# Performance work log

Hardware: AMD Instinct MI355X
Metric: run time of the kernel (lower is better)

Reference implementation:

```python
import jax, jax.numpy as jnp
import numpy as np
from jax import lax

B, C_IN, H, W = 128, 3, 256, 256
C_OUT, K = 16, 3


def setup_inputs() -> dict:
    key = jax.random.key(0)
    k1, k2, k3 = jax.random.split(key, 3)
    x = jax.random.normal(k1, (B, C_IN, H, W), dtype=jnp.float32)
    # PyTorch ConvTranspose2d weight layout: (in_channels, out_channels, kH, kW)
    weight = jax.random.normal(k2, (C_IN, C_OUT, K, K), dtype=jnp.float32) * (1.0 / np.sqrt(C_IN * K * K))
    bias = jax.random.normal(k3, (C_OUT, 1, 1), dtype=jnp.float32)
    return {"x": x, "weight": weight, "bias": bias}


def reference(x, weight, bias):
    # conv_transpose2d(stride=1, padding=0) == full correlation with spatially
    # flipped kernel, with in/out channel axes swapped to OIHW.
    k = weight.shape[-1]
    w = jnp.flip(weight, axis=(2, 3)).transpose(1, 0, 2, 3)  # [C_out, C_in, k, k]
    y = lax.conv_general_dilated(
        x, w,
        window_strides=(1, 1),
        padding=[(k - 1, k - 1), (k - 1, k - 1)],
        dimension_numbers=("NCHW", "OIHW", "NCHW"),
    )  # [B, C_out, H+k-1, W+k-1]
    y = jnp.mean(y, axis=(2, 3), keepdims=True)          # [B, C_out, 1, 1]
    y = y + bias[None]                                   # broadcast [C_out,1,1]
    y = jax.nn.logsumexp(y, axis=1, keepdims=True)       # [B, 1, 1, 1]
    y = jnp.sum(y, axis=(2, 3))                          # [B, 1]
    return y * 10.0
```

## Files before the change

### kernel.cpp

```cpp
#include <hip/hip_runtime.h>

#define BATCH   128
#define C_IN    3
#define C_OUT   16
#define HW      65536
#define F4_PER_PLANE 16384
#define THREADS 1024
#define NWAVES  (THREADS / 64)
#define F4_ITERS (F4_PER_PLANE / THREADS)

__global__ __launch_bounds__(THREADS) void fused_batch(
        const float* __restrict__ x,
        const float* __restrict__ weight,
        const float* __restrict__ bias,
        float* __restrict__ out) {
    const int b = blockIdx.x;
    const int t = threadIdx.x;
    const float4* xp = (const float4*)x + (size_t)b * (3 * F4_PER_PLANE);

    float a0 = 0.0f, a1 = 0.0f, a2 = 0.0f;
#pragma unroll
    for (int i = 0; i < F4_ITERS; ++i) {
        float4 v0 = xp[0 * F4_PER_PLANE + i * THREADS + t];
        float4 v1 = xp[1 * F4_PER_PLANE + i * THREADS + t];
        float4 v2 = xp[2 * F4_PER_PLANE + i * THREADS + t];
        a0 += (v0.x + v0.y) + (v0.z + v0.w);
        a1 += (v1.x + v1.y) + (v1.z + v1.w);
        a2 += (v2.x + v2.y) + (v2.z + v2.w);
    }

#pragma unroll
    for (int off = 32; off > 0; off >>= 1) {
        a0 += __shfl_down(a0, off, 64);
        a1 += __shfl_down(a1, off, 64);
        a2 += __shfl_down(a2, off, 64);
    }
    __shared__ float smem[NWAVES][3];
    const int lane = t & 63;
    const int wv   = t >> 6;
    if (lane == 0) { smem[wv][0] = a0; smem[wv][1] = a1; smem[wv][2] = a2; }
    __syncthreads();

    if (t == 0) {
        float S[C_IN] = {0.0f, 0.0f, 0.0f};
#pragma unroll
        for (int w = 0; w < NWAVES; ++w) {
            S[0] += smem[w][0];
            S[1] += smem[w][1];
            S[2] += smem[w][2];
        }
        const float inv_area = 1.0f / (258.0f * 258.0f);
        float m[C_OUT];
        float mmax = -1e30f;
#pragma unroll
        for (int co = 0; co < C_OUT; ++co) {
            float v = bias[co];
#pragma unroll
            for (int ci = 0; ci < C_IN; ++ci) {
                float ws9 = 0.0f;
#pragma unroll
                for (int k = 0; k < 9; ++k)
                    ws9 += weight[(ci * C_OUT + co) * 9 + k];
                v += S[ci] * ws9 * inv_area;
            }
            m[co] = v;
            mmax = fmaxf(mmax, v);
        }
        float se = 0.0f;
#pragma unroll
        for (int co = 0; co < C_OUT; ++co) se += expf(m[co] - mmax);
        out[b] = 10.0f * (logf(se) + mmax);
    }
}

extern "C" void kernel_launch(void* const* d_in, const int* in_sizes, int n_in,
                              void* d_out, int out_size, void* d_ws, size_t ws_size,
                              hipStream_t stream) {
    const float* x      = (const float*)d_in[0];
    const float* weight = (const float*)d_in[1];
    const float* bias   = (const float*)d_in[2];
    float* out = (float*)d_out;

    fused_batch<<<BATCH, THREADS, 0, stream>>>(x, weight, bias, out);
}
```

Measured before the change: 150.9 us.

## Split each batch reduction across two blocks with atomic last-block finalize

Each batch's spatial sum is now computed by two blocks, each covering half of every plane, which doubles the grid from 128 to 256 blocks. Each block writes its partial channel sums to workspace and bumps a per-batch atomic counter. The second block to arrive combines the two partials and runs the logsumexp epilogue. The goal is to fill more of the GPU's compute units for this memory-bound reduction, at the cost of an extra memset launch and atomic/fence traffic.

```diff
diff --git a/kernel.cpp b/kernel.cpp
--- a/kernel.cpp
+++ b/kernel.cpp
@@ -3,24 +3,31 @@
 #define BATCH   128
 #define C_IN    3
 #define C_OUT   16
-#define HW      65536
 #define F4_PER_PLANE 16384
 #define THREADS 1024
 #define NWAVES  (THREADS / 64)
-#define F4_ITERS (F4_PER_PLANE / THREADS)
+#define NBLK    (BATCH * 2)
+#define F4_HALF (F4_PER_PLANE / 2)
+#define ITERS   (F4_HALF / THREADS)
 
-__global__ __launch_bounds__(THREADS) void fused_batch(
+#define CNT_OFF 1024
+#define CNT_STRIDE 16
+
+__global__ __launch_bounds__(THREADS) void fused_pair(
         const float* __restrict__ x,
         const float* __restrict__ weight,
         const float* __restrict__ bias,
+        float* __restrict__ ws,
         float* __restrict__ out) {
-    const int b = blockIdx.x;
-    const int t = threadIdx.x;
-    const float4* xp = (const float4*)x + (size_t)b * (3 * F4_PER_PLANE);
+    const int b    = blockIdx.x >> 1;
+    const int half = blockIdx.x & 1;
+    const int t    = threadIdx.x;
+    const float4* xp = (const float4*)x
+                     + (size_t)b * (3 * F4_PER_PLANE) + half * F4_HALF;
 
     float a0 = 0.0f, a1 = 0.0f, a2 = 0.0f;
 #pragma unroll
-    for (int i = 0; i < F4_ITERS; ++i) {
+    for (int i = 0; i < ITERS; ++i) {
         float4 v0 = xp[0 * F4_PER_PLANE + i * THREADS + t];
         float4 v1 = xp[1 * F4_PER_PLANE + i * THREADS + t];
         float4 v2 = xp[2 * F4_PER_PLANE + i * THREADS + t];
@@ -41,36 +48,46 @@
     if (lane == 0) { smem[wv][0] = a0; smem[wv][1] = a1; smem[wv][2] = a2; }
     __syncthreads();
 
-    if (t == 0) {
-        float S[C_IN] = {0.0f, 0.0f, 0.0f};
+    if (t != 0) return;
+
+    float S0 = 0.0f, S1 = 0.0f, S2 = 0.0f;
 #pragma unroll
-        for (int w = 0; w < NWAVES; ++w) {
-            S[0] += smem[w][0];
-            S[1] += smem[w][1];
-            S[2] += smem[w][2];
+    for (int w = 0; w < NWAVES; ++w) {
+        S0 += smem[w][0]; S1 += smem[w][1]; S2 += smem[w][2];
+    }
+
+    float* slot = ws + blockIdx.x * 4;
+    slot[0] = S0; slot[1] = S1; slot[2] = S2;
+    __threadfence();
+    unsigned* cnt = (unsigned*)(ws + CNT_OFF) + b * CNT_STRIDE;
+    unsigned prev = atomicAdd(cnt, 1u);
+    if (prev != 1u) return;
+
+    __threadfence();
+    const float* pslot = ws + (blockIdx.x ^ 1) * 4;
+    S0 += pslot[0]; S1 += pslot[1]; S2 += pslot[2];
+
+    const float inv_area = 1.0f / (258.0f * 258.0f);
+    float m[C_OUT];
+    float mmax = -1e30f;
+#pragma unroll
+    for (int co = 0; co < C_OUT; ++co) {
+        float v = bias[co];
+        float w0 = 0.0f, w1 = 0.0f, w2 = 0.0f;
+#pragma unroll
+        for (int k = 0; k < 9; ++k) {
+            w0 += weight[(0 * C_OUT + co) * 9 + k];
+            w1 += weight[(1 * C_OUT + co) * 9 + k];
+            w2 += weight[(2 * C_OUT + co) * 9 + k];
         }
-        const float inv_area = 1.0f / (258.0f * 258.0f);
-        float m[C_OUT];
-        float mmax = -1e30f;
+        v += (S0 * w0 + S1 * w1 + S2 * w2) * inv_area;
+        m[co] = v;
+        mmax = fmaxf(mmax, v);
+    }
+    float se = 0.0f;
 #pragma unroll
-        for (int co = 0; co < C_OUT; ++co) {
-            float v = bias[co];
-#pragma unroll
-            for (int ci = 0; ci < C_IN; ++ci) {
-                float ws9 = 0.0f;
-#pragma unroll
-                for (int k = 0; k < 9; ++k)
-                    ws9 += weight[(ci * C_OUT + co) * 9 + k];
-                v += S[ci] * ws9 * inv_area;
-            }
-            m[co] = v;
-            mmax = fmaxf(mmax, v);
-        }
-        float se = 0.0f;
-#pragma unroll
-        for (int co = 0; co < C_OUT; ++co) se += expf(m[co] - mmax);
-        out[b] = 10.0f * (logf(se) + mmax);
-    }
+    for (int co = 0; co < C_OUT; ++co) se += expf(m[co] - mmax);
+    out[b] = 10.0f * (logf(se) + mmax);
 }
 
 extern "C" void kernel_launch(void* const* d_in, const int* in_sizes, int n_in,
@@ -80,6 +97,8 @@
     const float* weight = (const float*)d_in[1];
     const float* bias   = (const float*)d_in[2];
     float* out = (float*)d_out;
+    float* ws  = (float*)d_ws;
 
-    fused_batch<<<BATCH, THREADS, 0, stream>>>(x, weight, bias, out);
+    hipMemsetAsync(ws + CNT_OFF, 0, BATCH * CNT_STRIDE * sizeof(unsigned), stream);
+    fused_pair<<<NBLK, THREADS, 0, stream>>>(x, weight, bias, ws, out);
 }
```

Result: slower. 160.6 us (+6.4%).
